# Performance work log

Measured on AMD Instinct MI355X. Metric: run time of the kernel, lower is better.

## Reference

```python
import jax, jax.numpy as jnp
import numpy as np

DIM = 768
HEADS = 12
HD = DIM // HEADS  # 64
BASE = 100.0


def rope_sincos(H, W):
    # DINOv3 RopePositionEmbedding: normalize_coords='separate', base=100.0
    dd = HD // 4
    periods = BASE ** (jnp.arange(dd, dtype=jnp.float32) / dd)          # [dd]
    ch = (jnp.arange(H, dtype=jnp.float32) + 0.5) / H                    # pixel centers
    cw = (jnp.arange(W, dtype=jnp.float32) + 0.5) / W
    cy, cx = jnp.meshgrid(ch, cw, indexing='ij')
    coords = 2.0 * jnp.stack([cy, cx], axis=-1).reshape(H * W, 2) - 1.0  # [N,2] in [-1,1]
    angles = 2.0 * jnp.pi * coords[:, :, None] / periods[None, None, :]  # [N,2,dd]
    angles = angles.reshape(H * W, 2 * dd)                               # [N, HD//2]
    angles = jnp.concatenate([angles, angles], axis=-1)                  # [N, HD]
    return jnp.sin(angles), jnp.cos(angles)


def rotate_half(t):
    t1, t2 = jnp.split(t, 2, axis=-1)
    return jnp.concatenate([-t2, t1], axis=-1)


def setup_inputs() -> dict:
    key = jax.random.key(0)
    k1, k2, k3 = jax.random.split(key, 3)
    B, H, W = 2, 48, 48
    x = jax.random.normal(k1, (B, H, W, DIM), dtype=jnp.float32)
    w_qkv = jax.random.normal(k2, (3 * DIM, DIM), dtype=jnp.float32) * 0.02
    b_qkv = jnp.zeros((3 * DIM,), dtype=jnp.float32)
    w_proj = jax.random.normal(k3, (DIM, DIM), dtype=jnp.float32) * 0.02
    b_proj = jnp.zeros((DIM,), dtype=jnp.float32)
    return {"x": x, "w_qkv": w_qkv, "b_qkv": b_qkv, "w_proj": w_proj, "b_proj": b_proj}


def reference(x, w_qkv, b_qkv, w_proj, b_proj):
    B, H, W, C = x.shape
    N = H * W
    xf = x.reshape(B, N, C)
    qkv = xf @ w_qkv.T + b_qkv                                   # [B,N,3C]
    qkv = qkv.reshape(B, N, 3, HEADS, HD).transpose(2, 0, 3, 1, 4)
    q, k, v = qkv[0], qkv[1], qkv[2]                              # [B,h,N,d]
    sin, cos = rope_sincos(H, W)                                  # [N,d]
    q = q * cos + rotate_half(q) * sin
    k = k * cos + rotate_half(k) * sin
    scale = HD ** -0.5
    attn = jax.nn.softmax(jnp.einsum('bhqd,bhkd->bhqk', q, k) * scale, axis=-1)
    o = jnp.einsum('bhqk,bhkd->bhqd', attn, v)                    # [B,h,N,d]
    o = o.transpose(0, 2, 1, 3).reshape(B, N, C)
    o = o @ w_proj.T + b_proj
    return o.reshape(B, H, W, C)
```

## Files before the change

kernel.cpp:

```cpp
#include <hip/hip_runtime.h>

#define BATCH 2
#define NSEQ 2304
#define DIM 768
#define HEADS 12
#define HD 64
#define M_TOK (BATCH * NSEQ)
#define LDSP 72
#define KP 72
#define BH (BATCH * HEADS)
#define KT_HALF (NSEQ / 64 / 2)
#define NKT (DIM / 64)

typedef __attribute__((ext_vector_type(8))) short bf16x8;
typedef __attribute__((ext_vector_type(8))) short short8v;
typedef __attribute__((ext_vector_type(4))) float f32x4;
typedef __fp16 fp16x2 __attribute__((ext_vector_type(2)));
typedef _Float16 half4 __attribute__((ext_vector_type(4)));
typedef _Float16 half8 __attribute__((ext_vector_type(8)));

#define QSCALE (0.125f * 1.44269504088896f)
#define LOG2_100_D16 0.41524101186092029f

__device__ __forceinline__ short f2bf(float f) {
    union { float f; unsigned u; } v; v.f = f;
    unsigned r = v.u + 0x7fffu + ((v.u >> 16) & 1u);
    return (short)(r >> 16);
}

#define CN1 (M_TOK * DIM / 4)
#define CN2 (3 * DIM * DIM / 4)
#define CN3 (DIM * DIM / 4)
__global__ void cvt_all_kernel(const float* __restrict__ x, const float* __restrict__ wq,
                               const float* __restrict__ wp,
                               short* __restrict__ xb, short* __restrict__ wqb,
                               short* __restrict__ wpb) {
    int i = blockIdx.x * 256 + threadIdx.x;
    const float* src; short* dst; int j;
    if (i < CN1)              { src = x;  dst = xb;  j = i; }
    else if (i < CN1 + CN2)   { src = wq; dst = wqb; j = i - CN1; }
    else                      { src = wp; dst = wpb; j = i - CN1 - CN2; }
    float4 v = reinterpret_cast<const float4*>(src)[j];
    short4 o;
    o.x = f2bf(v.x); o.y = f2bf(v.y); o.z = f2bf(v.z); o.w = f2bf(v.w);
    reinterpret_cast<short4*>(dst)[j] = o;
}

__global__ __launch_bounds__(512) void gemm_qkv_kernel(
    const short* __restrict__ A,
    const short* __restrict__ Bt,
    const float* __restrict__ bias,
    short* __restrict__ qb, short* __restrict__ kbuf, _Float16* __restrict__ vtb)
{
    __shared__ __align__(16) short At[2][128 * 64];
    __shared__ __align__(16) short Bl[2][128 * 64];
    const int m0 = blockIdx.x * 128, n0 = blockIdx.y * 128;
    const int tid = threadIdx.x, lane = tid & 63, wave = tid >> 6;
    const int quad = lane >> 4, l16 = lane & 15;
    const int wm = (wave >> 1) * 32, wn = (wave & 1) * 64;
    f32x4 acc[2][4] = {};

    const int lrow = lane >> 3;
    const int jsw = (lane & 7) ^ lrow;
    const short* aBase = &A[(size_t)(m0 + wave * 16 + lrow) * DIM + jsw * 8];
    const short* bBase = &Bt[(size_t)(n0 + wave * 16 + lrow) * DIM + jsw * 8];

    auto stage = [&](int buf, int k0) {
#pragma unroll
        for (int i = 0; i < 2; ++i) {
            __builtin_amdgcn_global_load_lds(
                (const __attribute__((address_space(1))) unsigned int*)(aBase + k0 + i * 8 * DIM),
                (__attribute__((address_space(3))) unsigned int*)&At[buf][(wave * 2 + i) * 512],
                16, 0, 0);
            __builtin_amdgcn_global_load_lds(
                (const __attribute__((address_space(1))) unsigned int*)(bBase + k0 + i * 8 * DIM),
                (__attribute__((address_space(3))) unsigned int*)&Bl[buf][(wave * 2 + i) * 512],
                16, 0, 0);
        }
    };

    stage(0, 0);

    const int rx = l16 & 7;
    int cur = 0;
    for (int kt = 0; kt < NKT; ++kt) {
        __syncthreads();
        if (kt + 1 < NKT) stage(cur ^ 1, (kt + 1) * 64);
#pragma unroll
        for (int ks = 0; ks < 2; ++ks) {
            bf16x8 af[2], bf[4];
#pragma unroll
            for (int mt = 0; mt < 2; ++mt) {
                const int R = wm + mt * 16 + l16;
                af[mt] = *reinterpret_cast<const bf16x8*>(
                    &At[cur][R * 64 + (((ks * 4 + quad) ^ rx) * 8)]);
            }
#pragma unroll
            for (int nt = 0; nt < 4; ++nt) {
                const int R = wn + nt * 16 + l16;
                bf[nt] = *reinterpret_cast<const bf16x8*>(
                    &Bl[cur][R * 64 + (((ks * 4 + quad) ^ rx) * 8)]);
            }
#pragma unroll
            for (int mt = 0; mt < 2; ++mt)
#pragma unroll
                for (int nt = 0; nt < 4; ++nt)
                    acc[mt][nt] = __builtin_amdgcn_mfma_f32_16x16x32_bf16(af[mt], bf[nt], acc[mt][nt], 0, 0, 0);
        }
        cur ^= 1;
    }

    const int which = (n0 + wn) / DIM;
    const int head = ((n0 + wn) % DIM) / HD;
    const int b = m0 / NSEQ;
    const int tokb = m0 % NSEQ + wm;
    if (which == 2) {
#pragma unroll
        for (int mt = 0; mt < 2; ++mt)
#pragma unroll
            for (int nt = 0; nt < 4; ++nt) {
                const int n = n0 + wn + nt * 16 + l16;
                const int d = nt * 16 + l16;
                const float bi = bias[n];
                const int tok0 = tokb + mt * 16 + quad * 4;
                half4 hv;
                hv.x = (_Float16)(acc[mt][nt][0] + bi);
                hv.y = (_Float16)(acc[mt][nt][1] + bi);
                hv.z = (_Float16)(acc[mt][nt][2] + bi);
                hv.w = (_Float16)(acc[mt][nt][3] + bi);
                *reinterpret_cast<half4*>(&vtb[((size_t)(b * HEADS + head) * HD + d) * NSEQ + tok0]) = hv;
            }
    } else {
        short* dst = (which == 0) ? qb : kbuf;
        const float qs = (which == 0) ? QSCALE : 1.0f;
        float bi[4];
#pragma unroll
        for (int nt = 0; nt < 4; ++nt) bi[nt] = bias[n0 + wn + nt * 16 + l16];
        const float invp = __builtin_amdgcn_exp2f(-(float)l16 * LOG2_100_D16);
#pragma unroll
        for (int mt = 0; mt < 2; ++mt) {
#pragma unroll
            for (int rg = 0; rg < 4; ++rg) {
                const int tok = tokb + mt * 16 + quad * 4 + rg;
                const int yy = tok / 48, xx = tok - yy * 48;
                const float ry = (2.0f * (yy + 0.5f) * (1.0f / 48.0f) - 1.0f) * invp;
                const float rx2 = (2.0f * (xx + 0.5f) * (1.0f / 48.0f) - 1.0f) * invp;
                const float sy = __builtin_amdgcn_sinf(ry), cy = __builtin_amdgcn_cosf(ry);
                const float sx = __builtin_amdgcn_sinf(rx2), cx = __builtin_amdgcn_cosf(rx2);
                const float a0 = acc[mt][0][rg] + bi[0];
                const float a1 = acc[mt][1][rg] + bi[1];
                const float a2 = acc[mt][2][rg] + bi[2];
                const float a3 = acc[mt][3][rg] + bi[3];
                short* rp = &dst[((size_t)(b * HEADS + head) * NSEQ + tok) * HD];
                rp[l16]      = f2bf((a0 * cy - a2 * sy) * qs);
                rp[32 + l16] = f2bf((a2 * cy + a0 * sy) * qs);
                rp[16 + l16] = f2bf((a1 * cx - a3 * sx) * qs);
                rp[48 + l16] = f2bf((a3 * cx + a1 * sx) * qs);
            }
        }
    }
}

__global__ __launch_bounds__(512, 4) void attn_kernel(
    const short* __restrict__ qb, const short* __restrict__ kb,
    const _Float16* __restrict__ vtb, _Float16* __restrict__ opart,
    float* __restrict__ lpart)
{
    __shared__ __align__(16) short    Kt[2][64 * KP];
    __shared__ __align__(16) _Float16 Vt[2][64 * KP];
    const int wg = blockIdx.x;
    const int xcd = wg & 7;
    const int slot = wg >> 3;
    const int slab = xcd * 6 + slot / 9;
    const int qt = slot % 9;
    const int kh = slab & 1;
    const int bh = slab >> 1;
    const int tid = threadIdx.x, lane = tid & 63, wave = tid >> 6;
    const int quad = lane >> 4, l16 = lane & 15;
    const int qrow0 = qt * 256 + wave * 32;
    const short* qbase = qb + (size_t)bh * NSEQ * HD;
    const short* kbase = kb + (size_t)bh * NSEQ * HD;
    const _Float16* vbase = vtb + (size_t)bh * HD * NSEQ;

    bf16x8 qf[2][2];
#pragma unroll
    for (int mt = 0; mt < 2; ++mt)
#pragma unroll
        for (int ks = 0; ks < 2; ++ks)
            qf[mt][ks] = *reinterpret_cast<const bf16x8*>(
                &qbase[(size_t)(qrow0 + mt * 16 + l16) * HD + ks * 32 + quad * 8]);

    half8 ones8;
#pragma unroll
    for (int j = 0; j < 8; ++j) ones8[j] = (_Float16)1.0f;

    f32x4 oacc[2][4] = {};
    f32x4 lacc[2] = {};

    const int rk = tid >> 3, ck = (tid & 7) * 8;
    const int wv = tid & 7;
    const int vdst = rk * KP + 32 * (wv >> 2) + 16 * (wv & 1) + 4 * ((wv >> 1) & 1);
    const int t0 = kh * (NSEQ / 2);
    const short* kp = kbase + (size_t)(t0 + rk) * HD + ck;
    const _Float16* vp = vbase + (size_t)rk * NSEQ + t0 + wv * 8;

    {
        uint4 k0 = *reinterpret_cast<const uint4*>(kp);
        uint4 v0 = *reinterpret_cast<const uint4*>(vp);
        *reinterpret_cast<uint4*>(&Kt[0][rk * KP + ck]) = k0;
        _Float16* vb = &Vt[0][vdst];
        *reinterpret_cast<uint2*>(vb + 0) = make_uint2(v0.x, v0.y);
        *reinterpret_cast<uint2*>(vb + 8) = make_uint2(v0.z, v0.w);
        kp += 64 * HD;
        vp += 64;
    }

    int cur = 0;
    for (int kt = 0; kt < KT_HALF; ++kt) {
        __syncthreads();
        uint4 k0, v0;
        const bool pre = (kt + 1 < KT_HALF);
        if (pre) {
            k0 = *reinterpret_cast<const uint4*>(kp);
            v0 = *reinterpret_cast<const uint4*>(vp);
            kp += 64 * HD;
            vp += 64;
        }

        bf16x8 kf[2][4];
#pragma unroll
        for (int ks = 0; ks < 2; ++ks)
#pragma unroll
            for (int nt = 0; nt < 4; ++nt)
                kf[ks][nt] = *reinterpret_cast<const bf16x8*>(
                    &Kt[cur][(nt * 16 + l16) * KP + ks * 32 + quad * 8]);
        half8 vf8[2][4];
#pragma unroll
        for (int n2 = 0; n2 < 2; ++n2)
#pragma unroll
            for (int dt = 0; dt < 4; ++dt)
                vf8[n2][dt] = *reinterpret_cast<const half8*>(
                    &Vt[cur][(dt * 16 + l16) * KP + 32 * n2 + 8 * quad]);

#pragma unroll
        for (int mt = 0; mt < 2; ++mt) {
            f32x4 sacc[4] = {};
#pragma unroll
            for (int ks = 0; ks < 2; ++ks)
#pragma unroll
                for (int nt = 0; nt < 4; ++nt)
                    sacc[nt] = __builtin_amdgcn_mfma_f32_16x16x32_bf16(
                        kf[ks][nt], qf[mt][ks], sacc[nt], 0, 0, 0);

            half8 pf8[2];
#pragma unroll
            for (int n2 = 0; n2 < 2; ++n2) {
                fp16x2 w0 = __builtin_amdgcn_cvt_pkrtz(
                    __builtin_amdgcn_exp2f(sacc[2 * n2][0]),
                    __builtin_amdgcn_exp2f(sacc[2 * n2][1]));
                fp16x2 w1 = __builtin_amdgcn_cvt_pkrtz(
                    __builtin_amdgcn_exp2f(sacc[2 * n2][2]),
                    __builtin_amdgcn_exp2f(sacc[2 * n2][3]));
                fp16x2 w2 = __builtin_amdgcn_cvt_pkrtz(
                    __builtin_amdgcn_exp2f(sacc[2 * n2 + 1][0]),
                    __builtin_amdgcn_exp2f(sacc[2 * n2 + 1][1]));
                fp16x2 w3 = __builtin_amdgcn_cvt_pkrtz(
                    __builtin_amdgcn_exp2f(sacc[2 * n2 + 1][2]),
                    __builtin_amdgcn_exp2f(sacc[2 * n2 + 1][3]));
                half8 p;
                p[0] = (_Float16)w0.x; p[1] = (_Float16)w0.y;
                p[2] = (_Float16)w1.x; p[3] = (_Float16)w1.y;
                p[4] = (_Float16)w2.x; p[5] = (_Float16)w2.y;
                p[6] = (_Float16)w3.x; p[7] = (_Float16)w3.y;
                pf8[n2] = p;
            }

#pragma unroll
            for (int n2 = 0; n2 < 2; ++n2)
                lacc[mt] = __builtin_amdgcn_mfma_f32_16x16x32_f16(
                    pf8[n2], ones8, lacc[mt], 0, 0, 0);
#pragma unroll
            for (int n2 = 0; n2 < 2; ++n2)
#pragma unroll
                for (int dt = 0; dt < 4; ++dt)
                    oacc[mt][dt] = __builtin_amdgcn_mfma_f32_16x16x32_f16(
                        pf8[n2], vf8[n2][dt], oacc[mt][dt], 0, 0, 0);
        }

        if (pre) {
            *reinterpret_cast<uint4*>(&Kt[cur ^ 1][rk * KP + ck]) = k0;
            _Float16* vb = &Vt[cur ^ 1][vdst];
            *reinterpret_cast<uint2*>(vb + 0) = make_uint2(v0.x, v0.y);
            *reinterpret_cast<uint2*>(vb + 8) = make_uint2(v0.z, v0.w);
        }
        cur ^= 1;
    }

    _Float16* ob2 = opart + (size_t)(kh * BH + bh) * NSEQ * HD;
    float* lp2 = lpart + (size_t)(kh * BH + bh) * NSEQ;
#pragma unroll
    for (int mt = 0; mt < 2; ++mt) {
#pragma unroll
        for (int dt = 0; dt < 4; ++dt)
#pragma unroll
            for (int rg = 0; rg < 4; ++rg) {
                int row = qrow0 + mt * 16 + quad * 4 + rg;
                ob2[(size_t)row * HD + dt * 16 + l16] = (_Float16)oacc[mt][dt][rg];
            }
        if (l16 == 0) {
#pragma unroll
            for (int rg = 0; rg < 4; ++rg)
                lp2[qrow0 + mt * 16 + quad * 4 + rg] = lacc[mt][rg];
        }
    }
}

__global__ __launch_bounds__(256) void gemm_proj_kernel(
    const _Float16* __restrict__ op,
    const float* __restrict__ lp,
    const short* __restrict__ Bt,
    const float* __restrict__ bias,
    float* __restrict__ out)
{
    __shared__ __align__(16) short At[64 * LDSP];
    __shared__ __align__(16) short Bl[64 * LDSP];
    const int m0 = blockIdx.x * 64, n0 = blockIdx.y * 64;
    const int tid = threadIdx.x, lane = tid & 63, wave = tid >> 6;
    const int quad = lane >> 4, l16 = lane & 15;
    const int wm = (wave >> 1) * 32, wn = (wave & 1) * 32;
    const int r = tid >> 2, cs = (tid & 3) * 16;
    const int b = m0 / NSEQ;
    const int tok = m0 % NSEQ + r;
    f32x4 acc[2][2] = {};

    for (int k0 = 0; k0 < DIM; k0 += 64) {
        const int h = k0 >> 6;
        const size_t pb = (size_t)(b * HEADS + h) * NSEQ + tok;
        const float l0 = lp[pb], l1 = lp[(size_t)BH * NSEQ + pb];
        const float inv = __builtin_amdgcn_rcpf(l0 + l1);
        const half8* o0 = reinterpret_cast<const half8*>(&op[pb * HD + cs]);
        const half8* o1 = reinterpret_cast<const half8*>(&op[(size_t)BH * NSEQ * HD + pb * HD + cs]);
        half8 p0 = o0[0], p1 = o0[1], q0 = o1[0], q1 = o1[1];
        const uint4* gb = reinterpret_cast<const uint4*>(&Bt[(size_t)(n0 + r) * DIM + k0 + cs]);
        uint4 bw0 = gb[0], bw1 = gb[1];
        short8v s0, s1;
#pragma unroll
        for (int j = 0; j < 8; ++j) {
            s0[j] = f2bf(((float)p0[j] + (float)q0[j]) * inv);
            s1[j] = f2bf(((float)p1[j] + (float)q1[j]) * inv);
        }
        *reinterpret_cast<short8v*>(&At[r * LDSP + cs]) = s0;
        *reinterpret_cast<short8v*>(&At[r * LDSP + cs + 8]) = s1;
        uint4* sb = reinterpret_cast<uint4*>(&Bl[r * LDSP + cs]);
        sb[0] = bw0; sb[1] = bw1;
        __syncthreads();
#pragma unroll
        for (int ks = 0; ks < 2; ++ks) {
            bf16x8 af[2], bf[2];
#pragma unroll
            for (int mt = 0; mt < 2; ++mt)
                af[mt] = *reinterpret_cast<const bf16x8*>(&At[(wm + mt * 16 + l16) * LDSP + ks * 32 + quad * 8]);
#pragma unroll
            for (int nt = 0; nt < 2; ++nt)
                bf[nt] = *reinterpret_cast<const bf16x8*>(&Bl[(wn + nt * 16 + l16) * LDSP + ks * 32 + quad * 8]);
#pragma unroll
            for (int mt = 0; mt < 2; ++mt)
#pragma unroll
                for (int nt = 0; nt < 2; ++nt)
                    acc[mt][nt] = __builtin_amdgcn_mfma_f32_16x16x32_bf16(af[mt], bf[nt], acc[mt][nt], 0, 0, 0);
        }
        __syncthreads();
    }

#pragma unroll
    for (int mt = 0; mt < 2; ++mt)
#pragma unroll
        for (int nt = 0; nt < 2; ++nt) {
            const int n = n0 + wn + nt * 16 + l16;
            const float bi = bias[n];
#pragma unroll
            for (int rg = 0; rg < 4; ++rg) {
                const int m = m0 + wm + mt * 16 + quad * 4 + rg;
                out[(size_t)m * DIM + n] = acc[mt][nt][rg] + bi;
            }
        }
}

extern "C" void kernel_launch(void* const* d_in, const int* in_sizes, int n_in,
                              void* d_out, int out_size, void* d_ws, size_t ws_size,
                              hipStream_t stream) {
    const float* x      = (const float*)d_in[0];
    const float* w_qkv  = (const float*)d_in[1];
    const float* b_qkv  = (const float*)d_in[2];
    const float* w_proj = (const float*)d_in[3];
    const float* b_proj = (const float*)d_in[4];
    float* out = (float*)d_out;

    short* xb     = (short*)d_ws;
    short* wqkvb  = xb + (size_t)M_TOK * DIM;
    short* wprojb = wqkvb + (size_t)3 * DIM * DIM;
    short* qb     = wprojb + (size_t)DIM * DIM;
    short* kb     = qb + (size_t)BH * NSEQ * HD;
    short* vtb    = kb + (size_t)BH * NSEQ * HD;
    short* opart  = vtb + (size_t)BH * NSEQ * HD;
    float* lpart  = (float*)(opart + (size_t)2 * BH * NSEQ * HD);

    cvt_all_kernel<<<(CN1 + CN2 + CN3) / 256, 256, 0, stream>>>(
        x, w_qkv, w_proj, xb, wqkvb, wprojb);

    dim3 g1(M_TOK / 128, 3 * DIM / 128);
    gemm_qkv_kernel<<<g1, 512, 0, stream>>>(xb, wqkvb, b_qkv, qb, kb, (_Float16*)vtb);

    attn_kernel<<<dim3(9 * 2 * BH), 512, 0, stream>>>(qb, kb, (const _Float16*)vtb,
                                                      (_Float16*)opart, lpart);

    gemm_proj_kernel<<<dim3(M_TOK / 64, DIM / 64), 256, 0, stream>>>(
        (const _Float16*)opart, lpart, wprojb, b_proj, out);
}
```

Baseline: 163.5 us.

## Double-buffer proj GEMM with async LDS loads and 128-row tiles

```diff
diff --git a/kernel.cpp b/kernel.cpp
--- a/kernel.cpp
+++ b/kernel.cpp
@@ -315,61 +315,90 @@
     }
 }
 
-__global__ __launch_bounds__(256) void gemm_proj_kernel(
+__global__ __launch_bounds__(512) void gemm_proj_kernel(
     const _Float16* __restrict__ op,
     const float* __restrict__ lp,
     const short* __restrict__ Bt,
     const float* __restrict__ bias,
     float* __restrict__ out)
 {
-    __shared__ __align__(16) short At[64 * LDSP];
-    __shared__ __align__(16) short Bl[64 * LDSP];
-    const int m0 = blockIdx.x * 64, n0 = blockIdx.y * 64;
+    __shared__ __align__(16) short At[2][128 * LDSP];
+    __shared__ __align__(16) short Bl[2][64 * 64];
+    const int m0 = blockIdx.x * 128, n0 = blockIdx.y * 64;
     const int tid = threadIdx.x, lane = tid & 63, wave = tid >> 6;
     const int quad = lane >> 4, l16 = lane & 15;
     const int wm = (wave >> 1) * 32, wn = (wave & 1) * 32;
-    const int r = tid >> 2, cs = (tid & 3) * 16;
     const int b = m0 / NSEQ;
-    const int tok = m0 % NSEQ + r;
+    const int ra = tid >> 2, ca = (tid & 3) * 16;
+    const int tok = m0 % NSEQ + ra;
     f32x4 acc[2][2] = {};
 
-    for (int k0 = 0; k0 < DIM; k0 += 64) {
-        const int h = k0 >> 6;
+    const int lrow = lane >> 3;
+    const int jsw = (lane & 7) ^ lrow;
+    const short* bBase = &Bt[(size_t)(n0 + wave * 8 + lrow) * DIM + jsw * 8];
+    auto stageB = [&](int buf, int k0) {
+        __builtin_amdgcn_global_load_lds(
+            (const __attribute__((address_space(1))) unsigned int*)(bBase + k0),
+            (__attribute__((address_space(3))) unsigned int*)&Bl[buf][wave * 512],
+            16, 0, 0);
+    };
+
+    half8 a0, a1, a2, a3;
+    float ls;
+    auto loadA = [&](int h) {
         const size_t pb = (size_t)(b * HEADS + h) * NSEQ + tok;
-        const float l0 = lp[pb], l1 = lp[(size_t)BH * NSEQ + pb];
-        const float inv = __builtin_amdgcn_rcpf(l0 + l1);
-        const half8* o0 = reinterpret_cast<const half8*>(&op[pb * HD + cs]);
-        const half8* o1 = reinterpret_cast<const half8*>(&op[(size_t)BH * NSEQ * HD + pb * HD + cs]);
-        half8 p0 = o0[0], p1 = o0[1], q0 = o1[0], q1 = o1[1];
-        const uint4* gb = reinterpret_cast<const uint4*>(&Bt[(size_t)(n0 + r) * DIM + k0 + cs]);
-        uint4 bw0 = gb[0], bw1 = gb[1];
+        const half8* o0 = reinterpret_cast<const half8*>(&op[pb * HD + ca]);
+        const half8* o1 = reinterpret_cast<const half8*>(&op[(size_t)BH * NSEQ * HD + pb * HD + ca]);
+        a0 = o0[0]; a1 = o0[1];
+        a2 = o1[0]; a3 = o1[1];
+        ls = lp[pb] + lp[(size_t)BH * NSEQ + pb];
+    };
+    auto storeA = [&](int buf) {
+        const float inv = __builtin_amdgcn_rcpf(ls);
         short8v s0, s1;
 #pragma unroll
         for (int j = 0; j < 8; ++j) {
-            s0[j] = f2bf(((float)p0[j] + (float)q0[j]) * inv);
-            s1[j] = f2bf(((float)p1[j] + (float)q1[j]) * inv);
-        }
-        *reinterpret_cast<short8v*>(&At[r * LDSP + cs]) = s0;
-        *reinterpret_cast<short8v*>(&At[r * LDSP + cs + 8]) = s1;
-        uint4* sb = reinterpret_cast<uint4*>(&Bl[r * LDSP + cs]);
-        sb[0] = bw0; sb[1] = bw1;
+            s0[j] = f2bf(((float)a0[j] + (float)a2[j]) * inv);
+            s1[j] = f2bf(((float)a1[j] + (float)a3[j]) * inv);
+        }
+        *reinterpret_cast<short8v*>(&At[buf][ra * LDSP + ca]) = s0;
+        *reinterpret_cast<short8v*>(&At[buf][ra * LDSP + ca + 8]) = s1;
+    };
+
+    loadA(0);
+    stageB(0, 0);
+    storeA(0);
+
+    const int rx = l16 & 7;
+    int cur = 0;
+    for (int t = 0; t < NKT; ++t) {
         __syncthreads();
+        const bool pre = (t + 1 < NKT);
+        if (pre) {
+            stageB(cur ^ 1, (t + 1) * 64);
+            loadA(t + 1);
+        }
 #pragma unroll
         for (int ks = 0; ks < 2; ++ks) {
             bf16x8 af[2], bf[2];
 #pragma unroll
             for (int mt = 0; mt < 2; ++mt)
-                af[mt] = *reinterpret_cast<const bf16x8*>(&At[(wm + mt * 16 + l16) * LDSP + ks * 32 + quad * 8]);
-#pragma unroll
-            for (int nt = 0; nt < 2; ++nt)
-                bf[nt] = *reinterpret_cast<const bf16x8*>(&Bl[(wn + nt * 16 + l16) * LDSP + ks * 32 + quad * 8]);
+                af[mt] = *reinterpret_cast<const bf16x8*>(
+                    &At[cur][(wm + mt * 16 + l16) * LDSP + ks * 32 + quad * 8]);
+#pragma unroll
+            for (int nt = 0; nt < 2; ++nt) {
+                const int R = wn + nt * 16 + l16;
+                bf[nt] = *reinterpret_cast<const bf16x8*>(
+                    &Bl[cur][R * 64 + (((ks * 4 + quad) ^ rx) * 8)]);
+            }
 #pragma unroll
             for (int mt = 0; mt < 2; ++mt)
 #pragma unroll
                 for (int nt = 0; nt < 2; ++nt)
                     acc[mt][nt] = __builtin_amdgcn_mfma_f32_16x16x32_bf16(af[mt], bf[nt], acc[mt][nt], 0, 0, 0);
         }
-        __syncthreads();
+        if (pre) storeA(cur ^ 1);
+        cur ^= 1;
     }
 
 #pragma unroll
@@ -414,6 +443,6 @@
     attn_kernel<<<dim3(9 * 2 * BH), 512, 0, stream>>>(qb, kb, (const _Float16*)vtb,
                                                       (_Float16*)opart, lpart);
 
-    gemm_proj_kernel<<<dim3(M_TOK / 64, DIM / 64), 256, 0, stream>>>(
+    gemm_proj_kernel<<<dim3(M_TOK / 128, DIM / 64), 512, 0, stream>>>(
         (const _Float16*)opart, lpart, wprojb, b_proj, out);
 }
```

Result: no change. 165.0 us (+0.9%).
